# Kernel tuning notes

Hardware: AMD Instinct MI355X
Metric: run time of the kernel (lower is better)

Reference implementation:

```python
import jax, jax.numpy as jnp
import numpy as np

T, H, E, I, K = 4096, 2048, 8, 1408, 2


def setup_inputs() -> dict:
    key = jax.random.key(0)
    k1, k2, k3, k4 = jax.random.split(key, 4)
    x = jax.random.normal(k1, (T, H), dtype=jnp.float32)
    router_w = jax.random.normal(k2, (H, E), dtype=jnp.float32) * 0.02
    gate_up_proj = jax.random.normal(k3, (E, H, 2 * I), dtype=jnp.float32) * 0.02
    down_proj = jax.random.normal(k4, (E, I, H), dtype=jnp.float32) * 0.02
    return {"x": x, "router_w": router_w, "gate_up_proj": gate_up_proj, "down_proj": down_proj}


def _moe_forward(x, router_w, gate_up_proj, down_proj):
    # --- Router: softmax over experts, top-k selection (Qwen2-MoE style) ---
    logits = x @ router_w                                  # [T, E]
    probs = jax.nn.softmax(logits, axis=-1)
    topk_w, topk_idx = jax.lax.top_k(probs, K)             # [T, K]

    # --- Permute: replicate tokens per selected expert, stable-sort by expert id ---
    flat_eid = topk_idx.reshape(-1)                        # [T*K]
    rep_x = jnp.repeat(x, K, axis=0)                       # [T*K, H]
    sort_idx = jnp.argsort(flat_eid, stable=True)          # token permute (like ops.permute)
    perm_x = rep_x[sort_idx]                               # [T*K, H] grouped by expert
    perm_eid = flat_eid[sort_idx]                          # [T*K]

    # --- Grouped expert MLP (gate_up GEMM -> SiLU*up -> down GEMM) ---
    # Faithful to grouped-GEMM math; expressed as a fixed loop over E experts
    # with row masking to stay jit-compatible (no data-dependent shapes).
    out = jnp.zeros_like(perm_x)
    for e in range(E):
        gu = perm_x @ gate_up_proj[e]                      # [T*K, 2I]
        gate, up = gu[:, :I], gu[:, I:]
        h = (jax.nn.silu(gate) * up) @ down_proj[e]        # [T*K, H]
        out = out + jnp.where((perm_eid == e)[:, None], h, 0.0)

    # --- Unpermute + weighted combine over top-k ---
    inv_sort = jnp.argsort(sort_idx)                       # inverse permute mapping
    unperm = out[inv_sort].reshape(T, K, H)
    return jnp.einsum('tkh,tk->th', unperm, topk_w)        # [T, H]


def reference(x, router_w, gate_up_proj, down_proj):
    return _moe_forward(x, router_w, gate_up_proj, down_proj)
```

## Files before the change

### kernel.cpp

```cpp
#include <hip/hip_runtime.h>
#include <hip/hip_bf16.h>

#define T_TOK 4096
#define H_DIM 2048
#define E_NUM 8
#define I_DIM 1408
#define RTOT  8192
#define MAXTILES 72

typedef __bf16 bf16x8 __attribute__((ext_vector_type(8)));
typedef float  floatx4 __attribute__((ext_vector_type(4)));

__device__ __forceinline__ unsigned short f2bf(float f) {
  union { float f; unsigned u; } v; v.f = f;
  unsigned r = v.u + 0x7FFFu + ((v.u >> 16) & 1u);
  return (unsigned short)(r >> 16);
}

__device__ __forceinline__ void async16(const void* g, void* l) {
  __builtin_amdgcn_global_load_lds(
      (__attribute__((address_space(1))) void*)(g),
      (__attribute__((address_space(3))) void*)(l), 16, 0, 0);
}

__global__ void router_kernel(const float* __restrict__ x, const float* __restrict__ rw,
                              int* __restrict__ topk_idx, float* __restrict__ topk_w,
                              int* __restrict__ counts) {
  int wave = threadIdx.x >> 6, lane = threadIdx.x & 63;
  int t = blockIdx.x * 4 + wave;
  const float* xr = x + (size_t)t * H_DIM;
  float acc[E_NUM];
#pragma unroll
  for (int e = 0; e < E_NUM; e++) acc[e] = 0.f;
  for (int h = lane; h < H_DIM; h += 64) {
    float xv = xr[h];
    const float* wr = rw + h * E_NUM;
#pragma unroll
    for (int e = 0; e < E_NUM; e++) acc[e] += xv * wr[e];
  }
#pragma unroll
  for (int e = 0; e < E_NUM; e++) {
    float v = acc[e];
#pragma unroll
    for (int s = 32; s > 0; s >>= 1) v += __shfl_xor(v, s, 64);
    acc[e] = v;
  }
  if (lane == 0) {
    float mx = acc[0];
#pragma unroll
    for (int e = 1; e < E_NUM; e++) mx = fmaxf(mx, acc[e]);
    float p[E_NUM], s = 0.f;
#pragma unroll
    for (int e = 0; e < E_NUM; e++) { p[e] = __expf(acc[e] - mx); s += p[e]; }
    float inv = 1.0f / s;
    int i0 = 0;
#pragma unroll
    for (int e = 1; e < E_NUM; e++) if (p[e] > p[i0]) i0 = e;
    int i1 = (i0 == 0) ? 1 : 0;
#pragma unroll
    for (int e = 0; e < E_NUM; e++) if (e != i0 && p[e] > p[i1]) i1 = e;
    topk_idx[t * 2]     = i0;
    topk_idx[t * 2 + 1] = i1;
    topk_w[t * 2]       = p[i0] * inv;
    topk_w[t * 2 + 1]   = p[i1] * inv;
    atomicAdd(&counts[i0], 1);
    atomicAdd(&counts[i1], 1);
  }
}

__global__ void scan_kernel(const int* __restrict__ counts, int* __restrict__ offsets,
                            int* __restrict__ cursors, int* __restrict__ tile_e,
                            int* __restrict__ tile_m0, int* __restrict__ tile_end) {
  if (threadIdx.x == 0) {
    int o = 0, nt = 0;
    for (int e = 0; e < E_NUM; e++) {
      offsets[e] = o; cursors[e] = o;
      int c = counts[e];
      for (int m = 0; m < c; m += 128) {
        tile_e[nt] = e; tile_m0[nt] = o + m; tile_end[nt] = o + c; nt++;
      }
      o += c;
    }
    for (; nt < MAXTILES; nt++) tile_e[nt] = -1;
  }
}

__global__ void assign_kernel(const int* __restrict__ topk_idx, const float* __restrict__ topk_w,
                              int* __restrict__ cursors, int* __restrict__ row_of,
                              int* __restrict__ tok_of, float* __restrict__ w_of) {
  int i = blockIdx.x * blockDim.x + threadIdx.x;
  int e = topk_idx[i];
  int row = atomicAdd(&cursors[e], 1);
  row_of[i] = row;
  tok_of[row] = i >> 1;
  w_of[row] = topk_w[i];
}

__global__ void gather_kernel(const float* __restrict__ x, const int* __restrict__ tok_of,
                              unsigned short* __restrict__ Xp) {
  int row = blockIdx.x;
  int t = tok_of[row];
  const float4* src = (const float4*)(x + (size_t)t * H_DIM);
  ushort4* dst = (ushort4*)(Xp + (size_t)row * H_DIM);
  for (int i = threadIdx.x; i < H_DIM / 4; i += 256) {
    float4 v = src[i];
    ushort4 o;
    o.x = f2bf(v.x); o.y = f2bf(v.y); o.z = f2bf(v.z); o.w = f2bf(v.w);
    dst[i] = o;
  }
}

__global__ void convert_gu_kernel(const float* __restrict__ W,
                                  unsigned short* __restrict__ WgT,
                                  unsigned short* __restrict__ WuT) {
  __shared__ float tile[32][33];
  int e = blockIdx.z;
  int k0 = blockIdx.y * 32;
  int n0 = blockIdx.x * 32;
  const float* Wp = W + (size_t)e * H_DIM * (2 * I_DIM);
  int tx = threadIdx.x & 31, ty = threadIdx.x >> 5;
#pragma unroll
  for (int i = 0; i < 4; i++) {
    int k = ty + i * 8;
    tile[k][tx] = Wp[(size_t)(k0 + k) * (2 * I_DIM) + n0 + tx];
  }
  __syncthreads();
  unsigned short* Op;
  int nb = n0;
  if (n0 < I_DIM) Op = WgT + (size_t)e * I_DIM * H_DIM;
  else { Op = WuT + (size_t)e * I_DIM * H_DIM; nb = n0 - I_DIM; }
#pragma unroll
  for (int i = 0; i < 4; i++) {
    int n = ty + i * 8;
    Op[(size_t)(nb + n) * H_DIM + k0 + tx] = f2bf(tile[tx][n]);
  }
}

__global__ void convert_dn_kernel(const float* __restrict__ W,
                                  unsigned short* __restrict__ WdT) {
  __shared__ float tile[32][33];
  int e = blockIdx.z;
  int k0 = blockIdx.y * 32;
  int n0 = blockIdx.x * 32;
  const float* Wp = W + (size_t)e * I_DIM * H_DIM;
  int tx = threadIdx.x & 31, ty = threadIdx.x >> 5;
#pragma unroll
  for (int i = 0; i < 4; i++) {
    int k = ty + i * 8;
    tile[k][tx] = Wp[(size_t)(k0 + k) * H_DIM + n0 + tx];
  }
  __syncthreads();
  unsigned short* Op = WdT + (size_t)e * H_DIM * I_DIM;
#pragma unroll
  for (int i = 0; i < 4; i++) {
    int n = ty + i * 8;
    Op[(size_t)(n0 + n) * I_DIM + k0 + tx] = f2bf(tile[tx][n]);
  }
}

__global__ __launch_bounds__(256, 2) void gemm1_kernel(
    const unsigned short* __restrict__ Xp,
    const unsigned short* __restrict__ WgT,
    const unsigned short* __restrict__ WuT,
    const int* __restrict__ tile_e, const int* __restrict__ tile_m0,
    const int* __restrict__ tile_end,
    unsigned short* __restrict__ Hmid) {
  int bid = blockIdx.x;
  int xcd = bid & 7, j = bid >> 3;
  int mt, n;
  if (j < 88) {
    int c = j / 44, jj = j % 44;
    n = jj >> 2;
    mt = xcd * 9 + c * 4 + (jj & 3);
  } else {
    mt = xcd * 9 + 8;
    n = j - 88;
  }
  int e = tile_e[mt];
  if (e < 0) return;
  int m0 = tile_m0[mt];
  int row_end = tile_end[mt];
  int n0 = n * 128;

  __shared__ unsigned short sA[128 * 32];
  __shared__ unsigned short sBg[128 * 32];
  __shared__ unsigned short sBu[128 * 32];

  int tid = threadIdx.x;
  int wave = tid >> 6, lane = tid & 63;

  const unsigned short* ga[2];
  const unsigned short* ggt[2];
  const unsigned short* gut[2];
  unsigned short *la[2], *lg[2], *lu[2];
  const size_t wbase = (size_t)e * I_DIM * H_DIM;
#pragma unroll
  for (int r = 0; r < 2; r++) {
    int lin = r * 256 + tid;
    int row = lin >> 2;
    int col = (lin & 3) * 8;
    int am = m0 + row; if (am > RTOT - 1) am = RTOT - 1;
    ga[r]  = Xp  + (size_t)am * H_DIM + col;
    ggt[r] = WgT + wbase + (size_t)(n0 + row) * H_DIM + col;
    gut[r] = WuT + wbase + (size_t)(n0 + row) * H_DIM + col;
    la[r] = sA  + lin * 8;
    lg[r] = sBg + lin * 8;
    lu[r] = sBu + lin * 8;
  }

  floatx4 accg[4][4] = {};
  floatx4 accu[4][4] = {};

  const unsigned short* sAb = sA  + ((wave & 1) * 64 + (lane & 15)) * 32 + (lane >> 4) * 8;
  const unsigned short* sGb = sBg + ((wave >> 1) * 64 + (lane & 15)) * 32 + (lane >> 4) * 8;
  const unsigned short* sUb = sBu + ((wave >> 1) * 64 + (lane & 15)) * 32 + (lane >> 4) * 8;

  for (int kb = 0; kb < H_DIM / 32; kb++) {
    __syncthreads();
#pragma unroll
    for (int r = 0; r < 2; r++) {
      async16(ga[r],  la[r]); ga[r]  += 32;
      async16(ggt[r], lg[r]); ggt[r] += 32;
      async16(gut[r], lu[r]); gut[r] += 32;
    }
    __syncthreads();
    bf16x8 a[4];
#pragma unroll
    for (int mi = 0; mi < 4; mi++) a[mi] = *(const bf16x8*)(sAb + mi * 16 * 32);
#pragma unroll
    for (int ni = 0; ni < 4; ni++) {
      bf16x8 bg = *(const bf16x8*)(sGb + ni * 16 * 32);
      bf16x8 bu = *(const bf16x8*)(sUb + ni * 16 * 32);
#pragma unroll
      for (int mi = 0; mi < 4; mi++) {
        accg[mi][ni] = __builtin_amdgcn_mfma_f32_16x16x32_bf16(a[mi], bg, accg[mi][ni], 0, 0, 0);
        accu[mi][ni] = __builtin_amdgcn_mfma_f32_16x16x32_bf16(a[mi], bu, accu[mi][ni], 0, 0, 0);
      }
    }
  }

  int mrow = m0 + (wave & 1) * 64 + (lane >> 4) * 4;
  int ncol = n0 + (wave >> 1) * 64 + (lane & 15);
#pragma unroll
  for (int mi = 0; mi < 4; mi++) {
#pragma unroll
    for (int r = 0; r < 4; r++) {
      int m = mrow + mi * 16 + r;
      if (m < row_end) {
        size_t base = (size_t)m * I_DIM + ncol;
#pragma unroll
        for (int ni = 0; ni < 4; ni++) {
          float g = accg[mi][ni][r];
          float u = accu[mi][ni][r];
          float s = g / (1.0f + __expf(-g));
          Hmid[base + ni * 16] = f2bf(s * u);
        }
      }
    }
  }
}

__global__ __launch_bounds__(256, 2) void gemm2_kernel(
    const unsigned short* __restrict__ Hmid,
    const unsigned short* __restrict__ WdT,
    const int* __restrict__ tile_e, const int* __restrict__ tile_m0,
    const int* __restrict__ tile_end,
    const int* __restrict__ tok_of, const float* __restrict__ w_of,
    float* __restrict__ out) {
  int bid = blockIdx.x;
  int xcd = bid & 7, j = bid >> 3;
  int mt, n;
  if (j < 128) {
    int c = j / 64, jj = j % 64;
    n = jj >> 2;
    mt = xcd * 9 + c * 4 + (jj & 3);
  } else {
    mt = xcd * 9 + 8;
    n = j - 128;
  }
  int e = tile_e[mt];
  if (e < 0) return;
  int m0 = tile_m0[mt];
  int row_end = tile_end[mt];
  int n0 = n * 128;

  __shared__ unsigned short sA[128 * 32];
  __shared__ unsigned short sB[128 * 32];

  int tid = threadIdx.x;
  int wave = tid >> 6, lane = tid & 63;

  const unsigned short* ga[2];
  const unsigned short* gb[2];
  unsigned short *la[2], *lb[2];
  const size_t wbase = (size_t)e * H_DIM * I_DIM;
#pragma unroll
  for (int r = 0; r < 2; r++) {
    int lin = r * 256 + tid;
    int row = lin >> 2;
    int col = (lin & 3) * 8;
    int am = m0 + row; if (am > RTOT - 1) am = RTOT - 1;
    ga[r] = Hmid + (size_t)am * I_DIM + col;
    gb[r] = WdT + wbase + (size_t)(n0 + row) * I_DIM + col;
    la[r] = sA + lin * 8;
    lb[r] = sB + lin * 8;
  }

  floatx4 acc[4][4] = {};

  const unsigned short* sAb = sA + ((wave & 1) * 64 + (lane & 15)) * 32 + (lane >> 4) * 8;
  const unsigned short* sBb = sB + ((wave >> 1) * 64 + (lane & 15)) * 32 + (lane >> 4) * 8;

  for (int kb = 0; kb < I_DIM / 32; kb++) {
    __syncthreads();
#pragma unroll
    for (int r = 0; r < 2; r++) {
      async16(ga[r], la[r]); ga[r] += 32;
      async16(gb[r], lb[r]); gb[r] += 32;
    }
    __syncthreads();
    bf16x8 a[4];
#pragma unroll
    for (int mi = 0; mi < 4; mi++) a[mi] = *(const bf16x8*)(sAb + mi * 16 * 32);
#pragma unroll
    for (int ni = 0; ni < 4; ni++) {
      bf16x8 b = *(const bf16x8*)(sBb + ni * 16 * 32);
#pragma unroll
      for (int mi = 0; mi < 4; mi++)
        acc[mi][ni] = __builtin_amdgcn_mfma_f32_16x16x32_bf16(a[mi], b, acc[mi][ni], 0, 0, 0);
    }
  }

  int mrow = m0 + (wave & 1) * 64 + (lane >> 4) * 4;
  int ncol = n0 + (wave >> 1) * 64 + (lane & 15);
#pragma unroll
  for (int mi = 0; mi < 4; mi++) {
#pragma unroll
    for (int r = 0; r < 4; r++) {
      int m = mrow + mi * 16 + r;
      if (m < row_end) {
        int t = tok_of[m];
        float w = w_of[m];
        float* op = out + (size_t)t * H_DIM + ncol;
#pragma unroll
        for (int ni = 0; ni < 4; ni++)
          atomicAdd(op + ni * 16, w * acc[mi][ni][r]);
      }
    }
  }
}

extern "C" void kernel_launch(void* const* d_in, const int* in_sizes, int n_in,
                              void* d_out, int out_size, void* d_ws, size_t ws_size,
                              hipStream_t stream) {
  const float* x   = (const float*)d_in[0];
  const float* rw  = (const float*)d_in[1];
  const float* wgu = (const float*)d_in[2];
  const float* wdn = (const float*)d_in[3];
  float* out = (float*)d_out;

  char* ws = (char*)d_ws;
  size_t off = 0;
  auto alloc = [&](size_t b) {
    char* p = ws + off;
    off = (off + b + 255) & ~(size_t)255;
    return p;
  };
  unsigned short* WgT  = (unsigned short*)alloc((size_t)E_NUM * I_DIM * H_DIM * 2);
  unsigned short* WuT  = (unsigned short*)alloc((size_t)E_NUM * I_DIM * H_DIM * 2);
  unsigned short* WdT  = (unsigned short*)alloc((size_t)E_NUM * H_DIM * I_DIM * 2);
  unsigned short* Xp   = (unsigned short*)alloc((size_t)RTOT * H_DIM * 2);
  unsigned short* Hmid = (unsigned short*)alloc((size_t)RTOT * I_DIM * 2);
  int*   topk_idx      = (int*)alloc(RTOT * 4);
  float* topk_w        = (float*)alloc(RTOT * 4);
  int*   row_of        = (int*)alloc(RTOT * 4);
  int*   tok_of        = (int*)alloc(RTOT * 4);
  float* w_of          = (float*)alloc(RTOT * 4);
  int*   counts        = (int*)alloc(256);
  int*   offsets       = (int*)alloc(256);
  int*   cursors       = (int*)alloc(256);
  int*   tile_e        = (int*)alloc(128 * 4);
  int*   tile_m0       = (int*)alloc(128 * 4);
  int*   tile_end      = (int*)alloc(128 * 4);

  hipMemsetAsync(counts, 0, E_NUM * sizeof(int), stream);
  hipMemsetAsync(d_out, 0, (size_t)out_size * sizeof(float), stream);

  convert_gu_kernel<<<dim3(88, 64, 8), 256, 0, stream>>>(wgu, WgT, WuT);
  convert_dn_kernel<<<dim3(64, 44, 8), 256, 0, stream>>>(wdn, WdT);
  router_kernel<<<T_TOK / 4, 256, 0, stream>>>(x, rw, topk_idx, topk_w, counts);
  scan_kernel<<<1, 64, 0, stream>>>(counts, offsets, cursors, tile_e, tile_m0, tile_end);
  assign_kernel<<<RTOT / 256, 256, 0, stream>>>(topk_idx, topk_w, cursors, row_of, tok_of, w_of);
  gather_kernel<<<RTOT, 256, 0, stream>>>(x, tok_of, Xp);
  gemm1_kernel<<<8 * 9 * 11, 256, 0, stream>>>(Xp, WgT, WuT, tile_e, tile_m0, tile_end, Hmid);
  gemm2_kernel<<<8 * 9 * 16, 256, 0, stream>>>(Hmid, WdT, tile_e, tile_m0, tile_end, tok_of, w_of, out);
}
```

Baseline: 789.1 us.

## Replace atomic scatter with dense H2 store plus combine; vectorize weight conversion

The down-projection GEMM now writes its fp32 results densely per permuted row into a workspace buffer instead of atomically adding weighted values into the output. A new combine kernel gathers each token's two rows and forms the weighted sum, which also removes the output memset. The weight transpose/convert kernels switch to 64x64 tiles with float4 loads, conversion to bf16 before the shared-memory stage, and ushort4 stores. The combine path costs an extra 64MB fp32 write and read plus one more launch, in exchange for removing atomic contention and gaining deterministic accumulation.

New measurement: 777.2 us. Within noise of the previous version (-1.5%).

```diff
diff --git a/kernel.cpp b/kernel.cpp
--- a/kernel.cpp
+++ b/kernel.cpp
@@ -85,15 +85,13 @@
   }
 }
 
-__global__ void assign_kernel(const int* __restrict__ topk_idx, const float* __restrict__ topk_w,
-                              int* __restrict__ cursors, int* __restrict__ row_of,
-                              int* __restrict__ tok_of, float* __restrict__ w_of) {
+__global__ void assign_kernel(const int* __restrict__ topk_idx, int* __restrict__ cursors,
+                              int* __restrict__ row_of, int* __restrict__ tok_of) {
   int i = blockIdx.x * blockDim.x + threadIdx.x;
   int e = topk_idx[i];
   int row = atomicAdd(&cursors[e], 1);
   row_of[i] = row;
   tok_of[row] = i >> 1;
-  w_of[row] = topk_w[i];
 }
 
 __global__ void gather_kernel(const float* __restrict__ x, const int* __restrict__ tok_of,
@@ -113,48 +111,58 @@
 __global__ void convert_gu_kernel(const float* __restrict__ W,
                                   unsigned short* __restrict__ WgT,
                                   unsigned short* __restrict__ WuT) {
-  __shared__ float tile[32][33];
+  __shared__ unsigned short t[64][72];
   int e = blockIdx.z;
-  int k0 = blockIdx.y * 32;
-  int n0 = blockIdx.x * 32;
+  int k0 = blockIdx.y * 64;
+  int n0 = blockIdx.x * 64;
   const float* Wp = W + (size_t)e * H_DIM * (2 * I_DIM);
-  int tx = threadIdx.x & 31, ty = threadIdx.x >> 5;
-#pragma unroll
-  for (int i = 0; i < 4; i++) {
-    int k = ty + i * 8;
-    tile[k][tx] = Wp[(size_t)(k0 + k) * (2 * I_DIM) + n0 + tx];
+  int f4 = threadIdx.x & 15, kr = threadIdx.x >> 4;
+#pragma unroll
+  for (int p = 0; p < 4; p++) {
+    int k = kr + p * 16;
+    float4 v = *(const float4*)(Wp + (size_t)(k0 + k) * (2 * I_DIM) + n0 + f4 * 4);
+    t[f4 * 4 + 0][k] = f2bf(v.x);
+    t[f4 * 4 + 1][k] = f2bf(v.y);
+    t[f4 * 4 + 2][k] = f2bf(v.z);
+    t[f4 * 4 + 3][k] = f2bf(v.w);
   }
   __syncthreads();
   unsigned short* Op;
   int nb = n0;
   if (n0 < I_DIM) Op = WgT + (size_t)e * I_DIM * H_DIM;
   else { Op = WuT + (size_t)e * I_DIM * H_DIM; nb = n0 - I_DIM; }
-#pragma unroll
-  for (int i = 0; i < 4; i++) {
-    int n = ty + i * 8;
-    Op[(size_t)(nb + n) * H_DIM + k0 + tx] = f2bf(tile[tx][n]);
+  int c = threadIdx.x & 15, nr = threadIdx.x >> 4;
+#pragma unroll
+  for (int p = 0; p < 4; p++) {
+    int n = nr + p * 16;
+    *(ushort4*)(Op + (size_t)(nb + n) * H_DIM + k0 + c * 4) = *(const ushort4*)&t[n][c * 4];
   }
 }
 
 __global__ void convert_dn_kernel(const float* __restrict__ W,
                                   unsigned short* __restrict__ WdT) {
-  __shared__ float tile[32][33];
+  __shared__ unsigned short t[64][72];
   int e = blockIdx.z;
-  int k0 = blockIdx.y * 32;
-  int n0 = blockIdx.x * 32;
+  int k0 = blockIdx.y * 64;
+  int n0 = blockIdx.x * 64;
   const float* Wp = W + (size_t)e * I_DIM * H_DIM;
-  int tx = threadIdx.x & 31, ty = threadIdx.x >> 5;
-#pragma unroll
-  for (int i = 0; i < 4; i++) {
-    int k = ty + i * 8;
-    tile[k][tx] = Wp[(size_t)(k0 + k) * H_DIM + n0 + tx];
+  int f4 = threadIdx.x & 15, kr = threadIdx.x >> 4;
+#pragma unroll
+  for (int p = 0; p < 4; p++) {
+    int k = kr + p * 16;
+    float4 v = *(const float4*)(Wp + (size_t)(k0 + k) * H_DIM + n0 + f4 * 4);
+    t[f4 * 4 + 0][k] = f2bf(v.x);
+    t[f4 * 4 + 1][k] = f2bf(v.y);
+    t[f4 * 4 + 2][k] = f2bf(v.z);
+    t[f4 * 4 + 3][k] = f2bf(v.w);
   }
   __syncthreads();
   unsigned short* Op = WdT + (size_t)e * H_DIM * I_DIM;
-#pragma unroll
-  for (int i = 0; i < 4; i++) {
-    int n = ty + i * 8;
-    Op[(size_t)(n0 + n) * I_DIM + k0 + tx] = f2bf(tile[tx][n]);
+  int c = threadIdx.x & 15, nr = threadIdx.x >> 4;
+#pragma unroll
+  for (int p = 0; p < 4; p++) {
+    int n = nr + p * 16;
+    *(ushort4*)(Op + (size_t)(n0 + n) * I_DIM + k0 + c * 4) = *(const ushort4*)&t[n][c * 4];
   }
 }
 
@@ -265,8 +273,7 @@
     const unsigned short* __restrict__ WdT,
     const int* __restrict__ tile_e, const int* __restrict__ tile_m0,
     const int* __restrict__ tile_end,
-    const int* __restrict__ tok_of, const float* __restrict__ w_of,
-    float* __restrict__ out) {
+    float* __restrict__ H2) {
   int bid = blockIdx.x;
   int xcd = bid & 7, j = bid >> 3;
   int mt, n;
@@ -339,15 +346,29 @@
     for (int r = 0; r < 4; r++) {
       int m = mrow + mi * 16 + r;
       if (m < row_end) {
-        int t = tok_of[m];
-        float w = w_of[m];
-        float* op = out + (size_t)t * H_DIM + ncol;
-#pragma unroll
-        for (int ni = 0; ni < 4; ni++)
-          atomicAdd(op + ni * 16, w * acc[mi][ni][r]);
+        size_t base = (size_t)m * H_DIM + ncol;
+#pragma unroll
+        for (int ni = 0; ni < 4; ni++) H2[base + ni * 16] = acc[mi][ni][r];
       }
     }
   }
+}
+
+__global__ void combine_kernel(const float* __restrict__ H2, const int* __restrict__ row_of,
+                               const float* __restrict__ topk_w, float* __restrict__ out) {
+  int t = blockIdx.x >> 1;
+  int part = blockIdx.x & 1;
+  int c = part * 1024 + threadIdx.x * 4;
+  int r0 = row_of[t * 2], r1 = row_of[t * 2 + 1];
+  float w0 = topk_w[t * 2], w1 = topk_w[t * 2 + 1];
+  float4 a = *(const float4*)(H2 + (size_t)r0 * H_DIM + c);
+  float4 b = *(const float4*)(H2 + (size_t)r1 * H_DIM + c);
+  float4 o;
+  o.x = w0 * a.x + w1 * b.x;
+  o.y = w0 * a.y + w1 * b.y;
+  o.z = w0 * a.z + w1 * b.z;
+  o.w = w0 * a.w + w1 * b.w;
+  *(float4*)(out + (size_t)t * H_DIM + c) = o;
 }
 
 extern "C" void kernel_launch(void* const* d_in, const int* in_sizes, int n_in,
@@ -371,11 +392,11 @@
   unsigned short* WdT  = (unsigned short*)alloc((size_t)E_NUM * H_DIM * I_DIM * 2);
   unsigned short* Xp   = (unsigned short*)alloc((size_t)RTOT * H_DIM * 2);
   unsigned short* Hmid = (unsigned short*)alloc((size_t)RTOT * I_DIM * 2);
+  float* H2            = (float*)alloc((size_t)RTOT * H_DIM * 4);
   int*   topk_idx      = (int*)alloc(RTOT * 4);
   float* topk_w        = (float*)alloc(RTOT * 4);
   int*   row_of        = (int*)alloc(RTOT * 4);
   int*   tok_of        = (int*)alloc(RTOT * 4);
-  float* w_of          = (float*)alloc(RTOT * 4);
   int*   counts        = (int*)alloc(256);
   int*   offsets       = (int*)alloc(256);
   int*   cursors       = (int*)alloc(256);
@@ -384,14 +405,14 @@
   int*   tile_end      = (int*)alloc(128 * 4);
 
   hipMemsetAsync(counts, 0, E_NUM * sizeof(int), stream);
-  hipMemsetAsync(d_out, 0, (size_t)out_size * sizeof(float), stream);
-
-  convert_gu_kernel<<<dim3(88, 64, 8), 256, 0, stream>>>(wgu, WgT, WuT);
-  convert_dn_kernel<<<dim3(64, 44, 8), 256, 0, stream>>>(wdn, WdT);
+
+  convert_gu_kernel<<<dim3(44, 32, 8), 256, 0, stream>>>(wgu, WgT, WuT);
+  convert_dn_kernel<<<dim3(32, 22, 8), 256, 0, stream>>>(wdn, WdT);
   router_kernel<<<T_TOK / 4, 256, 0, stream>>>(x, rw, topk_idx, topk_w, counts);
   scan_kernel<<<1, 64, 0, stream>>>(counts, offsets, cursors, tile_e, tile_m0, tile_end);
-  assign_kernel<<<RTOT / 256, 256, 0, stream>>>(topk_idx, topk_w, cursors, row_of, tok_of, w_of);
+  assign_kernel<<<RTOT / 256, 256, 0, stream>>>(topk_idx, cursors, row_of, tok_of);
   gather_kernel<<<RTOT, 256, 0, stream>>>(x, tok_of, Xp);
   gemm1_kernel<<<8 * 9 * 11, 256, 0, stream>>>(Xp, WgT, WuT, tile_e, tile_m0, tile_end, Hmid);
-  gemm2_kernel<<<8 * 9 * 16, 256, 0, stream>>>(Hmid, WdT, tile_e, tile_m0, tile_end, tok_of, w_of, out);
-}
+  gemm2_kernel<<<8 * 9 * 16, 256, 0, stream>>>(Hmid, WdT, tile_e, tile_m0, tile_end, H2);
+  combine_kernel<<<T_TOK * 2, 256, 0, stream>>>(H2, row_of, topk_w, out);
+}
```
